# Performance work log

Hardware: AMD Instinct MI355X
Metric: run time of the kernel (lower is better)

## Reference

```python
import jax, jax.numpy as jnp
import numpy as np

U, I, D, L, NNZ = 8000, 16000, 64, 2, 768000
N = U + I


def setup_inputs() -> dict:
    key = jax.random.key(0)
    ks = jax.random.split(key, 10)
    return {
        "user_indices": jnp.arange(U, dtype=jnp.int64) if jax.config.jax_enable_x64 else jnp.arange(U, dtype=jnp.int32),
        "item_indices": jnp.arange(I, dtype=jnp.int32),
        "adj_rows": jax.random.randint(ks[0], (NNZ,), 0, N, dtype=jnp.int32),
        "adj_cols": jax.random.randint(ks[1], (NNZ,), 0, N, dtype=jnp.int32),
        "adj_vals": jax.random.uniform(ks[2], (NNZ,), dtype=jnp.float32),
        "user_emb": 0.1 * jax.random.normal(ks[3], (U, D), dtype=jnp.float32),
        "item_emb": 0.1 * jax.random.normal(ks[4], (I, D), dtype=jnp.float32),
        "gc_W": 0.05 * jax.random.normal(ks[5], (L, D, D), dtype=jnp.float32),
        "gc_b": jnp.zeros((L, D), dtype=jnp.float32),
        "bi_W": 0.05 * jax.random.normal(ks[6], (L, D, D), dtype=jnp.float32),
        "bi_b": jnp.zeros((L, D), dtype=jnp.float32),
    }


def reference(user_indices, item_indices, adj_rows, adj_cols, adj_vals,
              user_emb, item_emb, gc_W, gc_b, bi_W, bi_b):
    # embedding lookups + concat -> ego embeddings [N, D]
    ego = jnp.concatenate([user_emb[user_indices], item_emb[item_indices]], axis=0)
    n_nodes = ego.shape[0]
    all_embeddings = [ego]
    n_layers = gc_W.shape[0]
    for l in range(n_layers):
        # sparse.mm(adj, ego): gather neighbor rows, weight, scatter-add to rows
        side = jax.ops.segment_sum(adj_vals[:, None] * ego[adj_cols], adj_rows,
                                   num_segments=n_nodes)  # [N, D]
        sum_emb = jax.nn.leaky_relu(side @ gc_W[l].T + gc_b[l], negative_slope=0.01)
        bi_emb = jax.nn.leaky_relu((ego * side) @ bi_W[l].T + bi_b[l], negative_slope=0.01)
        ego = sum_emb + bi_emb
        all_embeddings.append(ego)
    all_emb = jnp.concatenate(all_embeddings, axis=1)  # [N, D*(L+1)]
    n_users = user_indices.shape[0]
    u_g = all_emb[:n_users]
    i_g = all_emb[n_users:]
    scores = u_g @ i_g.T  # [U, I]
    return jax.nn.log_softmax(scores, axis=1)
```

## Files before the change

kernel.cpp:

```cpp
#include <hip/hip_runtime.h>
#include <hip/hip_bf16.h>
#include <math.h>

#define NU   8000
#define NI   16000
#define NN   24000
#define DD   64
#define NL   2
#define NNZS 768000
#define KD   192
#define NCH  25
#define ACHUNK 640
#define CTILES 5
#define RBLK 63
#define CBLK 125

typedef __attribute__((ext_vector_type(8))) short  short8;
typedef __attribute__((ext_vector_type(4))) float  f32x4;

__device__ __forceinline__ unsigned short f2bf(float x) {
    union { float f; unsigned int u; } v; v.f = x;
    unsigned int r = v.u + 0x7fff + ((v.u >> 16) & 1);
    return (unsigned short)(r >> 16);
}
__device__ __forceinline__ float bf2f(unsigned short u) {
    union { unsigned int u; float f; } v; v.u = ((unsigned int)u) << 16;
    return v.f;
}

__device__ __forceinline__ int bslot(int nf, int kt, int g, int r16) {
    return ((((kt * 8 + nf) * 4 + g) * 16) + r16) ^ ((g + 4 * kt) & 7);
}

__global__ void k_concat(const int* __restrict__ uidx, const int* __restrict__ iidx,
                         const float* __restrict__ ue, const float* __restrict__ ie,
                         const float* __restrict__ gcW, const float* __restrict__ biW,
                         float* __restrict__ ego, unsigned short* __restrict__ allemb,
                         unsigned short* __restrict__ wbf, int* __restrict__ cnt) {
    int t = blockIdx.x * blockDim.x + threadIdx.x;
    if (t < NN) cnt[t] = 0;
    if (t < NL * DD * DD) {
        wbf[t] = f2bf(gcW[t]);
        wbf[NL * DD * DD + t] = f2bf(biW[t]);
    }
    if (t >= NN * DD) return;
    int n = t >> 6, d = t & 63;
    float v = (n < NU) ? ue[uidx[n] * DD + d] : ie[iidx[n - NU] * DD + d];
    ego[t] = v;
    allemb[(size_t)n * KD + d] = f2bf(v);
}

__global__ void k_hist(const int* __restrict__ rows, int* __restrict__ cnt) {
    int e = blockIdx.x * blockDim.x + threadIdx.x;
    if (e < NNZS) atomicAdd(&cnt[rows[e]], 1);
}

__global__ __launch_bounds__(1024) void k_scan(const int* __restrict__ cnt,
                                               int* __restrict__ rp, int* __restrict__ wp) {
    __shared__ int wsum[16];
    __shared__ int carry;
    int tid = threadIdx.x, lane = tid & 63, wid = tid >> 6;
    if (tid == 0) { carry = 0; rp[0] = 0; }
    __syncthreads();
    for (int base = 0; base < NN; base += 1024) {
        int i = base + tid;
        int v = (i < NN) ? cnt[i] : 0;
        int x = v;
#pragma unroll
        for (int off = 1; off < 64; off <<= 1) {
            int t = __shfl_up(x, off, 64);
            if (lane >= off) x += t;
        }
        if (lane == 63) wsum[wid] = x;
        __syncthreads();
        if (tid < 16) {
            int y = wsum[tid];
#pragma unroll
            for (int off = 1; off < 16; off <<= 1) {
                int t = __shfl_up(y, off, 64);
                if (tid >= off) y += t;
            }
            wsum[tid] = y;
        }
        __syncthreads();
        int blockoff = (wid == 0) ? 0 : wsum[wid - 1];
        int c = carry;
        int incl = c + blockoff + x;
        if (i < NN) { rp[i + 1] = incl; wp[i] = incl - v; }
        int total = wsum[15];
        __syncthreads();
        if (tid == 0) carry = c + total;
        __syncthreads();
    }
}

__global__ void k_scatter(const int* __restrict__ rows, const int* __restrict__ cols,
                          const float* __restrict__ vals, int* __restrict__ wp,
                          int2* __restrict__ edat) {
    int e = blockIdx.x * blockDim.x + threadIdx.x;
    if (e >= NNZS) return;
    int r = rows[e];
    int pos = atomicAdd(&wp[r], 1);
    edat[pos] = make_int2(cols[e], __float_as_int(vals[e]));
}

__global__ void k_spmm_csr(const int* __restrict__ rp, const int2* __restrict__ edat,
                           const unsigned short* __restrict__ feat, float* __restrict__ side) {
    int lane = threadIdx.x & 63;
    int wave = (blockIdx.x * blockDim.x + threadIdx.x) >> 6;
    int nw   = (gridDim.x * blockDim.x) >> 6;
    for (int r = wave; r < NN; r += nw) {
        int e0 = rp[r], e1 = rp[r + 1];
        float acc = 0.f;
        int e = e0;
        for (; e + 8 <= e1; e += 8) {
            int2 d[8];
#pragma unroll
            for (int j = 0; j < 8; ++j) d[j] = edat[e + j];
#pragma unroll
            for (int j = 0; j < 8; ++j)
                acc = fmaf(__int_as_float(d[j].y), bf2f(feat[(size_t)d[j].x * KD + lane]), acc);
        }
        for (; e < e1; ++e) {
            int2 d = edat[e];
            acc = fmaf(__int_as_float(d.y), bf2f(feat[(size_t)d.x * KD + lane]), acc);
        }
        side[(size_t)r * DD + lane] = acc;
    }
}

__global__ __launch_bounds__(256) void k_dense(const float* __restrict__ side, float* __restrict__ ego,
                        const unsigned short* __restrict__ wg_bf,
                        const unsigned short* __restrict__ wb_bf,
                        const float* __restrict__ gcb, const float* __restrict__ bib,
                        unsigned short* __restrict__ allemb, int colofs) {
    int lane = threadIdx.x & 63;
    int wave = threadIdx.x >> 6;
    int n0 = (blockIdx.x * 4 + wave) * 16;
    int nrow = lane & 15;
    int kofs = (lane >> 4) * 8;

    short8 bg[4][2], bb[4][2];
#pragma unroll
    for (int nf = 0; nf < 4; ++nf)
#pragma unroll
        for (int kt = 0; kt < 2; ++kt) {
            bg[nf][kt] = *(const short8*)(wg_bf + (nf * 16 + nrow) * DD + kt * 32 + kofs);
            bb[nf][kt] = *(const short8*)(wb_bf + (nf * 16 + nrow) * DD + kt * 32 + kofs);
        }

    short8 a1[2], a2[2];
    const float* sp = side + (size_t)(n0 + nrow) * DD;
    const float* ep = ego  + (size_t)(n0 + nrow) * DD;
#pragma unroll
    for (int kt = 0; kt < 2; ++kt) {
        int o = kt * 32 + kofs;
#pragma unroll
        for (int j = 0; j < 8; ++j) {
            float s = sp[o + j];
            float e = ep[o + j];
            a1[kt][j] = (short)f2bf(s);
            a2[kt][j] = (short)f2bf(e * s);
        }
    }

    f32x4 acc1[4], acc2[4];
#pragma unroll
    for (int nf = 0; nf < 4; ++nf) { acc1[nf] = (f32x4){0,0,0,0}; acc2[nf] = (f32x4){0,0,0,0}; }
#pragma unroll
    for (int nf = 0; nf < 4; ++nf)
#pragma unroll
        for (int kt = 0; kt < 2; ++kt) {
            acc1[nf] = __builtin_amdgcn_mfma_f32_16x16x32_bf16(a1[kt], bg[nf][kt], acc1[nf], 0, 0, 0);
            acc2[nf] = __builtin_amdgcn_mfma_f32_16x16x32_bf16(a2[kt], bb[nf][kt], acc2[nf], 0, 0, 0);
        }

    int g = lane >> 4;
#pragma unroll
    for (int nf = 0; nf < 4; ++nf) {
        int o = nf * 16 + nrow;
        float b1 = gcb[o], b2 = bib[o];
#pragma unroll
        for (int r = 0; r < 4; ++r) {
            int node = n0 + g * 4 + r;
            float v1 = acc1[nf][r] + b1;
            float v2 = acc2[nf][r] + b2;
            v1 = v1 > 0.f ? v1 : 0.01f * v1;
            v2 = v2 > 0.f ? v2 : 0.01f * v2;
            float v = v1 + v2;
            ego[(size_t)node * DD + o] = v;
            allemb[(size_t)node * KD + colofs + o] = f2bf(v);
        }
    }
}

__global__ __launch_bounds__(256) void k_lse_part(const unsigned short* __restrict__ allemb,
                                                  float* __restrict__ pm, float* __restrict__ ps) {
    __shared__ short8 Bs[3072];
    int id = blockIdx.x;
    int rowblk = id % RBLK;
    int chunk  = id / RBLK;
    int tid = threadIdx.x;
    int lane = tid & 63;
    int wave = tid >> 6;
    int r0 = rowblk * 128 + wave * 32;
    int c0 = chunk * ACHUNK;
    const unsigned short* A = allemb;
    const unsigned short* B = allemb + (size_t)NU * KD;
    int kofs = (lane >> 4) * 8;
    int g = lane >> 4;

    short8 a[2][6];
#pragma unroll
    for (int mi = 0; mi < 2; ++mi) {
        int ar = r0 + mi * 16 + (lane & 15);
        if (ar >= NU) ar = NU - 1;
#pragma unroll
        for (int kt = 0; kt < 6; ++kt)
            a[mi][kt] = *(const short8*)(A + (size_t)ar * KD + kt * 32 + kofs);
    }

    float m[2][4], s[2][4];
#pragma unroll
    for (int mi = 0; mi < 2; ++mi)
#pragma unroll
        for (int r = 0; r < 4; ++r) { m[mi][r] = -INFINITY; s[mi][r] = 0.f; }

    for (int t = 0; t < CTILES; ++t) {
        const unsigned short* Bt = B + (size_t)(c0 + t * 128) * KD;
        __syncthreads();
#pragma unroll
        for (int i = 0; i < 12; ++i) {
            int mm = i * 256 + tid;
            int r = mm / 24, c = mm - r * 24;
            int kt = c >> 2, gg = c & 3;
            Bs[bslot(r >> 4, kt, gg, r & 15)] = *(const short8*)(Bt + (size_t)r * KD + c * 8);
        }
        __syncthreads();

        f32x4 acc[2][8];
#pragma unroll
        for (int mi = 0; mi < 2; ++mi)
#pragma unroll
            for (int nf = 0; nf < 8; ++nf) acc[mi][nf] = (f32x4){0.f, 0.f, 0.f, 0.f};
#pragma unroll
        for (int nf = 0; nf < 8; ++nf)
#pragma unroll
            for (int kt = 0; kt < 6; ++kt) {
                short8 b = Bs[bslot(nf, kt, g, lane & 15)];
                acc[0][nf] = __builtin_amdgcn_mfma_f32_16x16x32_bf16(a[0][kt], b, acc[0][nf], 0, 0, 0);
                acc[1][nf] = __builtin_amdgcn_mfma_f32_16x16x32_bf16(a[1][kt], b, acc[1][nf], 0, 0, 0);
            }
#pragma unroll
        for (int mi = 0; mi < 2; ++mi)
#pragma unroll
            for (int r = 0; r < 4; ++r) {
                float lm = acc[mi][0][r];
#pragma unroll
                for (int nf = 1; nf < 8; ++nf) lm = fmaxf(lm, acc[mi][nf][r]);
                float nm = fmaxf(m[mi][r], lm);
                float p = 0.f;
#pragma unroll
                for (int nf = 0; nf < 8; ++nf) p += __expf(acc[mi][nf][r] - nm);
                s[mi][r] = s[mi][r] * __expf(m[mi][r] - nm) + p;
                m[mi][r] = nm;
            }
    }
#pragma unroll
    for (int mi = 0; mi < 2; ++mi)
#pragma unroll
        for (int r = 0; r < 4; ++r) {
            float mm = m[mi][r], ss = s[mi][r];
#pragma unroll
            for (int off = 1; off < 16; off <<= 1) {
                float om = __shfl_xor(mm, off, 64);
                float os = __shfl_xor(ss, off, 64);
                float nm = fmaxf(mm, om);
                ss = ss * __expf(mm - nm) + os * __expf(om - nm);
                mm = nm;
            }
            m[mi][r] = mm; s[mi][r] = ss;
        }
    if ((lane & 15) == 0) {
#pragma unroll
        for (int mi = 0; mi < 2; ++mi)
#pragma unroll
            for (int r = 0; r < 4; ++r) {
                int row = r0 + mi * 16 + g * 4 + r;
                if (row < NU) {
                    pm[chunk * NU + row] = m[mi][r];
                    ps[chunk * NU + row] = s[mi][r];
                }
            }
    }
}

__global__ void k_lse_comb(const float* __restrict__ pm, const float* __restrict__ ps,
                           float* __restrict__ lse) {
    int r = blockIdx.x * blockDim.x + threadIdx.x;
    if (r >= NU) return;
    float m = -INFINITY;
    for (int c = 0; c < NCH; ++c) m = fmaxf(m, pm[c * NU + r]);
    float s = 0.f;
    for (int c = 0; c < NCH; ++c) s += ps[c * NU + r] * __expf(pm[c * NU + r] - m);
    lse[r] = m + __logf(s);
}

__global__ __launch_bounds__(256) void k_out(const unsigned short* __restrict__ allemb,
                                             const float* __restrict__ lse, float* __restrict__ out) {
    __shared__ short8 Bs[3072];
    int id = blockIdx.x;
    int rowblk = id / CBLK;
    int colblk = id % CBLK;
    int tid = threadIdx.x;
    int lane = tid & 63;
    int wave = tid >> 6;
    int r0 = rowblk * 128 + wave * 32;
    int c0 = colblk * 128;
    const unsigned short* A = allemb;
    const unsigned short* B = allemb + (size_t)NU * KD;
    int kofs = (lane >> 4) * 8;
    int g = lane >> 4;

    const unsigned short* Bt = B + (size_t)c0 * KD;
#pragma unroll
    for (int i = 0; i < 12; ++i) {
        int mm = i * 256 + tid;
        int r = mm / 24, c = mm - r * 24;
        int kt = c >> 2, gg = c & 3;
        Bs[bslot(r >> 4, kt, gg, r & 15)] = *(const short8*)(Bt + (size_t)r * KD + c * 8);
    }

    short8 a[2][6];
#pragma unroll
    for (int mi = 0; mi < 2; ++mi) {
        int ar = r0 + mi * 16 + (lane & 15);
        if (ar >= NU) ar = NU - 1;
#pragma unroll
        for (int kt = 0; kt < 6; ++kt)
            a[mi][kt] = *(const short8*)(A + (size_t)ar * KD + kt * 32 + kofs);
    }
    float l4[2][4];
#pragma unroll
    for (int mi = 0; mi < 2; ++mi)
#pragma unroll
        for (int r = 0; r < 4; ++r) {
            int row = r0 + mi * 16 + g * 4 + r;
            l4[mi][r] = lse[row >= NU ? NU - 1 : row];
        }
    __syncthreads();

    f32x4 acc[2][8];
#pragma unroll
    for (int mi = 0; mi < 2; ++mi)
#pragma unroll
        for (int nf = 0; nf < 8; ++nf) acc[mi][nf] = (f32x4){0.f, 0.f, 0.f, 0.f};
#pragma unroll
    for (int nf = 0; nf < 8; ++nf)
#pragma unroll
        for (int kt = 0; kt < 6; ++kt) {
            short8 b = Bs[bslot(nf, kt, g, lane & 15)];
            acc[0][nf] = __builtin_amdgcn_mfma_f32_16x16x32_bf16(a[0][kt], b, acc[0][nf], 0, 0, 0);
            acc[1][nf] = __builtin_amdgcn_mfma_f32_16x16x32_bf16(a[1][kt], b, acc[1][nf], 0, 0, 0);
        }
    __syncthreads();

    float* tilef = (float*)Bs;
    float* tW = tilef + wave * 16 * 132;
#pragma unroll
    for (int mi = 0; mi < 2; ++mi) {
        int rowbase = r0 + mi * 16;
#pragma unroll
        for (int nf = 0; nf < 8; ++nf)
#pragma unroll
            for (int r = 0; r < 4; ++r)
                tW[(g * 4 + r) * 132 + nf * 16 + (lane & 15)] = acc[mi][nf][r] - l4[mi][r];
#pragma unroll
        for (int it = 0; it < 8; ++it) {
            int idx = it * 64 + lane;
            int rr = idx >> 5;
            int cc = (idx & 31) * 4;
            int row = rowbase + rr;
            if (row < NU) {
                f32x4 v = *(const f32x4*)&tW[rr * 132 + cc];
                __builtin_nontemporal_store(v, (f32x4*)&out[(size_t)row * NI + c0 + cc]);
            }
        }
    }
}

extern "C" void kernel_launch(void* const* d_in, const int* in_sizes, int n_in,
                              void* d_out, int out_size, void* d_ws, size_t ws_size,
                              hipStream_t stream) {
    const int*   uidx = (const int*)d_in[0];
    const int*   iidx = (const int*)d_in[1];
    const int*   arow = (const int*)d_in[2];
    const int*   acol = (const int*)d_in[3];
    const float* aval = (const float*)d_in[4];
    const float* ue   = (const float*)d_in[5];
    const float* ie   = (const float*)d_in[6];
    const float* gcW  = (const float*)d_in[7];
    const float* gcb  = (const float*)d_in[8];
    const float* biW  = (const float*)d_in[9];
    const float* bib  = (const float*)d_in[10];
    float* out = (float*)d_out;

    char* w = (char*)d_ws;
    float* ego  = (float*)w;                      w += (size_t)NN * DD * sizeof(float);
    float* side = (float*)w;                      w += (size_t)NN * DD * sizeof(float);
    unsigned short* allemb = (unsigned short*)w;  w += (size_t)NN * KD * sizeof(unsigned short);
    float* pm  = (float*)w;                       w += (size_t)NCH * NU * sizeof(float);
    float* ps  = (float*)w;                       w += (size_t)NCH * NU * sizeof(float);
    float* lse = (float*)w;                       w += (size_t)NU * sizeof(float);
    unsigned short* wbf = (unsigned short*)w;     w += (size_t)2 * NL * DD * DD * sizeof(unsigned short);
    int* cnt   = (int*)w;                         w += (size_t)NN * sizeof(int);
    int* rp    = (int*)w;                         w += (size_t)(NN + 4) * sizeof(int);
    int* wp    = (int*)w;                         w += (size_t)NN * sizeof(int);
    int2* edat = (int2*)w;                        w += (size_t)NNZS * sizeof(int2);

    unsigned short* wg_bf = wbf;
    unsigned short* wb_bf = wbf + NL * DD * DD;

    k_concat<<<(NN * DD + 255) / 256, 256, 0, stream>>>(uidx, iidx, ue, ie, gcW, biW,
                                                        ego, allemb, wbf, cnt);

    k_hist<<<(NNZS + 255) / 256, 256, 0, stream>>>(arow, cnt);
    k_scan<<<1, 1024, 0, stream>>>(cnt, rp, wp);
    k_scatter<<<(NNZS + 255) / 256, 256, 0, stream>>>(arow, acol, aval, wp, edat);

    for (int l = 0; l < NL; ++l) {
        k_spmm_csr<<<3000, 256, 0, stream>>>(rp, edat, allemb + l * DD, side);
        k_dense<<<NN / 64, 256, 0, stream>>>(side, ego, wg_bf + l * DD * DD, wb_bf + l * DD * DD,
                                             gcb + l * DD, bib + l * DD, allemb, (l + 1) * DD);
    }

    k_lse_part<<<RBLK * NCH, 256, 0, stream>>>(allemb, pm, ps);
    k_lse_comb<<<(NU + 255) / 256, 256, 0, stream>>>(pm, ps, lse);
    k_out<<<RBLK * CBLK, 256, 0, stream>>>(allemb, lse, out);
}
```

Measured before the change: 497.0 us.

## Fuse SpMM with dense layer via LDS and parallelize CSR prefix scan

Merges the CSR SpMM and dense MFMA layer into one kernel. Each wave gathers 16 rows of side into shared memory and then runs the bf16 MFMA transform directly, which removes the fp32 side and ego round trips through global memory. Ego is now read from the bf16 allemb copy instead of an fp32 buffer, which adds an extra rounding step. The single-block serial scan is replaced by a three-kernel multi-block scan. The fused kernel uses a fixed grid of NN/64 blocks, so it gives up the grid-stride balancing of the old SpMM.

After: 546.3 us. 1.1x slower.

```diff
diff --git a/kernel.cpp b/kernel.cpp
--- a/kernel.cpp
+++ b/kernel.cpp
@@ -14,6 +14,7 @@
 #define CTILES 5
 #define RBLK 63
 #define CBLK 125
+#define SCH  24
 
 typedef __attribute__((ext_vector_type(8))) short  short8;
 typedef __attribute__((ext_vector_type(4))) float  f32x4;
@@ -35,7 +36,7 @@
 __global__ void k_concat(const int* __restrict__ uidx, const int* __restrict__ iidx,
                          const float* __restrict__ ue, const float* __restrict__ ie,
                          const float* __restrict__ gcW, const float* __restrict__ biW,
-                         float* __restrict__ ego, unsigned short* __restrict__ allemb,
+                         unsigned short* __restrict__ allemb,
                          unsigned short* __restrict__ wbf, int* __restrict__ cnt) {
     int t = blockIdx.x * blockDim.x + threadIdx.x;
     if (t < NN) cnt[t] = 0;
@@ -46,7 +47,6 @@
     if (t >= NN * DD) return;
     int n = t >> 6, d = t & 63;
     float v = (n < NU) ? ue[uidx[n] * DD + d] : ie[iidx[n - NU] * DD + d];
-    ego[t] = v;
     allemb[(size_t)n * KD + d] = f2bf(v);
 }
 
@@ -55,43 +55,56 @@
     if (e < NNZS) atomicAdd(&cnt[rows[e]], 1);
 }
 
-__global__ __launch_bounds__(1024) void k_scan(const int* __restrict__ cnt,
-                                               int* __restrict__ rp, int* __restrict__ wp) {
+__global__ __launch_bounds__(1024) void k_scan1(const int* __restrict__ cnt,
+                                                int* __restrict__ rp, int* __restrict__ btot) {
     __shared__ int wsum[16];
-    __shared__ int carry;
     int tid = threadIdx.x, lane = tid & 63, wid = tid >> 6;
-    if (tid == 0) { carry = 0; rp[0] = 0; }
+    int i = blockIdx.x * 1024 + tid;
+    int v = (i < NN) ? cnt[i] : 0;
+    int x = v;
+#pragma unroll
+    for (int off = 1; off < 64; off <<= 1) {
+        int t = __shfl_up(x, off, 64);
+        if (lane >= off) x += t;
+    }
+    if (lane == 63) wsum[wid] = x;
     __syncthreads();
-    for (int base = 0; base < NN; base += 1024) {
-        int i = base + tid;
-        int v = (i < NN) ? cnt[i] : 0;
-        int x = v;
-#pragma unroll
-        for (int off = 1; off < 64; off <<= 1) {
-            int t = __shfl_up(x, off, 64);
-            if (lane >= off) x += t;
-        }
-        if (lane == 63) wsum[wid] = x;
-        __syncthreads();
-        if (tid < 16) {
-            int y = wsum[tid];
-#pragma unroll
-            for (int off = 1; off < 16; off <<= 1) {
-                int t = __shfl_up(y, off, 64);
-                if (tid >= off) y += t;
-            }
-            wsum[tid] = y;
-        }
-        __syncthreads();
-        int blockoff = (wid == 0) ? 0 : wsum[wid - 1];
-        int c = carry;
-        int incl = c + blockoff + x;
-        if (i < NN) { rp[i + 1] = incl; wp[i] = incl - v; }
-        int total = wsum[15];
-        __syncthreads();
-        if (tid == 0) carry = c + total;
-        __syncthreads();
-    }
+    if (tid < 16) {
+        int y = wsum[tid];
+#pragma unroll
+        for (int off = 1; off < 16; off <<= 1) {
+            int t = __shfl_up(y, off, 64);
+            if (tid >= off) y += t;
+        }
+        wsum[tid] = y;
+    }
+    __syncthreads();
+    int incl = x + (wid ? wsum[wid - 1] : 0);
+    if (i < NN) rp[i + 1] = incl;
+    if (tid == 0) btot[blockIdx.x] = wsum[15];
+}
+
+__global__ void k_scan2(const int* __restrict__ btot, int* __restrict__ boff) {
+    int tid = threadIdx.x;
+    int v = (tid < SCH) ? btot[tid] : 0;
+    int x = v;
+#pragma unroll
+    for (int off = 1; off < 32; off <<= 1) {
+        int t = __shfl_up(x, off, 64);
+        if (tid >= off) x += t;
+    }
+    if (tid < SCH) boff[tid] = x - v;
+}
+
+__global__ __launch_bounds__(1024) void k_scan3(const int* __restrict__ cnt,
+                                                const int* __restrict__ boff,
+                                                int* __restrict__ rp, int* __restrict__ wp) {
+    int i = blockIdx.x * 1024 + threadIdx.x;
+    if (i == 0) rp[0] = 0;
+    if (i >= NN) return;
+    int g = rp[i + 1] + boff[blockIdx.x];
+    rp[i + 1] = g;
+    wp[i] = g - cnt[i];
 }
 
 __global__ void k_scatter(const int* __restrict__ rows, const int* __restrict__ cols,
@@ -104,13 +117,19 @@
     edat[pos] = make_int2(cols[e], __float_as_int(vals[e]));
 }
 
-__global__ void k_spmm_csr(const int* __restrict__ rp, const int2* __restrict__ edat,
-                           const unsigned short* __restrict__ feat, float* __restrict__ side) {
-    int lane = threadIdx.x & 63;
-    int wave = (blockIdx.x * blockDim.x + threadIdx.x) >> 6;
-    int nw   = (gridDim.x * blockDim.x) >> 6;
-    for (int r = wave; r < NN; r += nw) {
-        int e0 = rp[r], e1 = rp[r + 1];
+__global__ __launch_bounds__(256) void k_layer(const int* __restrict__ rp, const int2* __restrict__ edat,
+                        unsigned short* __restrict__ allemb, int l,
+                        const unsigned short* __restrict__ wg_bf,
+                        const unsigned short* __restrict__ wb_bf,
+                        const float* __restrict__ gcb, const float* __restrict__ bib) {
+    __shared__ float sideS[4][16][66];
+    int tid = threadIdx.x, lane = tid & 63, wave = tid >> 6;
+    int n0 = blockIdx.x * 64 + wave * 16;
+    const unsigned short* feat = allemb + l * DD;
+
+    for (int k = 0; k < 16; ++k) {
+        int n = n0 + k;
+        int e0 = rp[n], e1 = rp[n + 1];
         float acc = 0.f;
         int e = e0;
         for (; e + 8 <= e1; e += 8) {
@@ -125,21 +144,10 @@
             int2 d = edat[e];
             acc = fmaf(__int_as_float(d.y), bf2f(feat[(size_t)d.x * KD + lane]), acc);
         }
-        side[(size_t)r * DD + lane] = acc;
-    }
-}
-
-__global__ __launch_bounds__(256) void k_dense(const float* __restrict__ side, float* __restrict__ ego,
-                        const unsigned short* __restrict__ wg_bf,
-                        const unsigned short* __restrict__ wb_bf,
-                        const float* __restrict__ gcb, const float* __restrict__ bib,
-                        unsigned short* __restrict__ allemb, int colofs) {
-    int lane = threadIdx.x & 63;
-    int wave = threadIdx.x >> 6;
-    int n0 = (blockIdx.x * 4 + wave) * 16;
-    int nrow = lane & 15;
-    int kofs = (lane >> 4) * 8;
-
+        sideS[wave][k][lane] = acc;
+    }
+
+    int nrow = lane & 15, kofs = (lane >> 4) * 8, g = lane >> 4;
     short8 bg[4][2], bb[4][2];
 #pragma unroll
     for (int nf = 0; nf < 4; ++nf)
@@ -150,15 +158,14 @@
         }
 
     short8 a1[2], a2[2];
-    const float* sp = side + (size_t)(n0 + nrow) * DD;
-    const float* ep = ego  + (size_t)(n0 + nrow) * DD;
+    const unsigned short* ep = feat + (size_t)(n0 + nrow) * KD;
 #pragma unroll
     for (int kt = 0; kt < 2; ++kt) {
         int o = kt * 32 + kofs;
 #pragma unroll
         for (int j = 0; j < 8; ++j) {
-            float s = sp[o + j];
-            float e = ep[o + j];
+            float s = sideS[wave][nrow][o + j];
+            float e = bf2f(ep[o + j]);
             a1[kt][j] = (short)f2bf(s);
             a2[kt][j] = (short)f2bf(e * s);
         }
@@ -175,7 +182,6 @@
             acc2[nf] = __builtin_amdgcn_mfma_f32_16x16x32_bf16(a2[kt], bb[nf][kt], acc2[nf], 0, 0, 0);
         }
 
-    int g = lane >> 4;
 #pragma unroll
     for (int nf = 0; nf < 4; ++nf) {
         int o = nf * 16 + nrow;
@@ -187,9 +193,7 @@
             float v2 = acc2[nf][r] + b2;
             v1 = v1 > 0.f ? v1 : 0.01f * v1;
             v2 = v2 > 0.f ? v2 : 0.01f * v2;
-            float v = v1 + v2;
-            ego[(size_t)node * DD + o] = v;
-            allemb[(size_t)node * KD + colofs + o] = f2bf(v);
+            allemb[(size_t)node * KD + (l + 1) * DD + o] = f2bf(v1 + v2);
         }
     }
 }
@@ -406,8 +410,6 @@
     float* out = (float*)d_out;
 
     char* w = (char*)d_ws;
-    float* ego  = (float*)w;                      w += (size_t)NN * DD * sizeof(float);
-    float* side = (float*)w;                      w += (size_t)NN * DD * sizeof(float);
     unsigned short* allemb = (unsigned short*)w;  w += (size_t)NN * KD * sizeof(unsigned short);
     float* pm  = (float*)w;                       w += (size_t)NCH * NU * sizeof(float);
     float* ps  = (float*)w;                       w += (size_t)NCH * NU * sizeof(float);
@@ -416,23 +418,26 @@
     int* cnt   = (int*)w;                         w += (size_t)NN * sizeof(int);
     int* rp    = (int*)w;                         w += (size_t)(NN + 4) * sizeof(int);
     int* wp    = (int*)w;                         w += (size_t)NN * sizeof(int);
+    int* btot  = (int*)w;                         w += 32 * sizeof(int);
+    int* boff  = (int*)w;                         w += 32 * sizeof(int);
     int2* edat = (int2*)w;                        w += (size_t)NNZS * sizeof(int2);
 
     unsigned short* wg_bf = wbf;
     unsigned short* wb_bf = wbf + NL * DD * DD;
 
     k_concat<<<(NN * DD + 255) / 256, 256, 0, stream>>>(uidx, iidx, ue, ie, gcW, biW,
-                                                        ego, allemb, wbf, cnt);
+                                                        allemb, wbf, cnt);
 
     k_hist<<<(NNZS + 255) / 256, 256, 0, stream>>>(arow, cnt);
-    k_scan<<<1, 1024, 0, stream>>>(cnt, rp, wp);
+    k_scan1<<<SCH, 1024, 0, stream>>>(cnt, rp, btot);
+    k_scan2<<<1, 64, 0, stream>>>(btot, boff);
+    k_scan3<<<SCH, 1024, 0, stream>>>(cnt, boff, rp, wp);
     k_scatter<<<(NNZS + 255) / 256, 256, 0, stream>>>(arow, acol, aval, wp, edat);
 
-    for (int l = 0; l < NL; ++l) {
-        k_spmm_csr<<<3000, 256, 0, stream>>>(rp, edat, allemb + l * DD, side);
-        k_dense<<<NN / 64, 256, 0, stream>>>(side, ego, wg_bf + l * DD * DD, wb_bf + l * DD * DD,
-                                             gcb + l * DD, bib + l * DD, allemb, (l + 1) * DD);
-    }
+    for (int l = 0; l < NL; ++l)
+        k_layer<<<NN / 64, 256, 0, stream>>>(rp, edat, allemb, l,
+                                             wg_bf + l * DD * DD, wb_bf + l * DD * DD,
+                                             gcb + l * DD, bib + l * DD);
 
     k_lse_part<<<RBLK * NCH, 256, 0, stream>>>(allemb, pm, ps);
     k_lse_comb<<<(NU + 255) / 256, 256, 0, stream>>>(pm, ps, lse);
```
